# Kernel tuning notes

Hardware: AMD Instinct MI355X
Metric: run time of the kernel (lower is better)

The kernel has to match this reference:

```python
import jax, jax.numpy as jnp
import numpy as np

N, S, R, M, C, CZ = 1, 128, 256, 256, 32, 128


def setup_inputs() -> dict:
    key = jax.random.key(0)
    k1, k2, k3, k4 = jax.random.split(key, 4)
    return {
        "msa_repr": jax.random.normal(k1, (N, S, R, M), dtype=jnp.float32) * 0.1,
        "left_w": jax.random.normal(k2, (M, C), dtype=jnp.float32) * 0.02,
        "right_w": jax.random.normal(k3, (M, C), dtype=jnp.float32) * 0.02,
        "out_w": jax.random.normal(k4, (C * C, CZ), dtype=jnp.float32) * 0.02,
    }


def reference(msa_repr, left_w, right_w, out_w):
    # msa_repr: [N,S,R,M]
    n, s, r, m = msa_repr.shape
    c = left_w.shape[1]
    # opm_projection: [N,S,R,M] @ [M,C] -> [N,S,R,C]
    left = jnp.einsum('nsrm,mc->nsrc', msa_repr, left_w)
    right = jnp.einsum('nsrm,mc->nsrc', msa_repr, right_w)
    # outer product summed over MSA dim s: [N,R,T,C,C]
    # (torch: a=left.transpose(-2,-3) -> [N,R,S,C]; einsum '...bac,...dae->...bdce')
    outer = jnp.einsum('nsrc,nste->nrtce', left, right).reshape(n, r, r, c * c)
    # project to pair channel: [N,R,T,C*C] @ [C*C,CZ] -> [N,R,T,CZ]
    return jnp.matmul(outer, out_w)
```

## Files before the change

### kernel.cpp

```cpp
#include <hip/hip_runtime.h>
#include <stdint.h>

#define S_DIM 128
#define R_DIM 256
#define M_DIM 256
#define C_DIM 32
#define CZ_DIM 128
#define K2_DIM 1024

typedef _Float16 f16;
typedef _Float16 f16x4 __attribute__((ext_vector_type(4)));
typedef _Float16 f16x8 __attribute__((ext_vector_type(8)));
typedef float f32x4 __attribute__((ext_vector_type(4)));
typedef float f32x16 __attribute__((ext_vector_type(16)));

typedef const __attribute__((address_space(1))) uint32_t gu32_t;
typedef __attribute__((address_space(3))) uint32_t lu32_t;
#define GLOAD_LDS16(g, l) \
    __builtin_amdgcn_global_load_lds((gu32_t*)(g), (lu32_t*)(l), 16, 0, 0)

__global__ __launch_bounds__(256, 4)
void proj_kernel(const float* __restrict__ msa, const float* __restrict__ lw,
                 const float* __restrict__ rw, const float* __restrict__ ow,
                 f16* __restrict__ left_t, f16* __restrict__ rt2,
                 f16* __restrict__ wt2) {
    __shared__ __align__(16) f16 wlT[8192];
    __shared__ __align__(16) f16 wrT[8192];

    int bid = blockIdx.x;
    int tid = threadIdx.x;
    int w = tid >> 6;
    int lane = tid & 63;
    int q = lane >> 4, li = lane & 15;
    int r  = bid >> 1;
    int s0 = (bid & 1) << 6;
    int s_col = s0 + w * 16 + li;

    const f32x4* bp = (const f32x4*)(msa + ((size_t)s_col * R_DIM + r) * M_DIM + q * 8);
    f32x4 b[16];
#pragma unroll
    for (int ks = 0; ks < 8; ks++) { b[2 * ks] = bp[ks * 8]; b[2 * ks + 1] = bp[ks * 8 + 1]; }

    {
        int i = bid * 256 + tid;
        int cz = i >> 10, k2 = i & 1023;
        int c = k2 >> 5, e = k2 & 31;
        int k2p = ((e >> 2) << 7) + (c << 2) + (e & 3);
        int ntile = cz >> 5, l31o = cz & 31;
        int kk = k2p >> 4, q5o = (k2p >> 3) & 1, j = k2p & 7;
        wt2[(ntile * 64 + kk) * 512 + (l31o * 2 + q5o) * 8 + j] = (f16)ow[k2 * CZ_DIM + cz];
    }
#pragma unroll
    for (int k = 0; k < 32; k++) {
        int i = k * 256 + tid;
        int m = i >> 5, c = i & 31;
        int d = ((m >> 3) * 32 + c) * 8 + (m & 7);
        wlT[d] = (f16)lw[i];
        wrT[d] = (f16)rw[i];
    }
    __syncthreads();

    f32x4 aL0 = {0,0,0,0}, aL1 = {0,0,0,0}, aR0 = {0,0,0,0}, aR1 = {0,0,0,0};
#pragma unroll
    for (int ks = 0; ks < 8; ks++) {
        f16x8 bf;
#pragma unroll
        for (int u = 0; u < 4; u++) { bf[u] = (f16)b[2*ks][u]; bf[4 + u] = (f16)b[2*ks+1][u]; }
        const f16* a0 = wlT + ((ks * 4 + q) * 32 + li) * 8;
        const f16* a1 = wrT + ((ks * 4 + q) * 32 + li) * 8;
        f16x8 al0 = *(const f16x8*)(a0);
        f16x8 al1 = *(const f16x8*)(a0 + 128);
        f16x8 ar0 = *(const f16x8*)(a1);
        f16x8 ar1 = *(const f16x8*)(a1 + 128);
        aL0 = __builtin_amdgcn_mfma_f32_16x16x32_f16(al0, bf, aL0, 0, 0, 0);
        aL1 = __builtin_amdgcn_mfma_f32_16x16x32_f16(al1, bf, aL1, 0, 0, 0);
        aR0 = __builtin_amdgcn_mfma_f32_16x16x32_f16(ar0, bf, aR0, 0, 0, 0);
        aR1 = __builtin_amdgcn_mfma_f32_16x16x32_f16(ar1, bf, aR1, 0, 0, 0);
    }
    int ks_s = s_col >> 4, q5_s = (s_col >> 3) & 1, j_s = s_col & 7;
    int sbase = (r * 8 + ks_s) * 512 + q5_s * 8 + j_s;
    int rl = r & 7;
    f16* Lb = left_t + (size_t)(r >> 3) * 32768;
    int sc = s_col >> 3, sj = s_col & 7;
#pragma unroll
    for (int reg = 0; reg < 4; reg++) {
        int c0 = q * 4 + reg;
        int row0 = rl * 32 + c0;
        int swz = sc ^ c0;
        Lb[(row0 * 16 + swz) * 8 + sj]        = (f16)aL0[reg];
        Lb[((row0 + 16) * 16 + swz) * 8 + sj] = (f16)aL1[reg];
        rt2[sbase + c0 * 16]        = (f16)aR0[reg];
        rt2[sbase + (c0 + 16) * 16] = (f16)aR1[reg];
    }
}

__global__ __launch_bounds__(512, 2)
void fuse_kernel(const f16* __restrict__ left_t, const f16* __restrict__ rt2,
                 const f16* __restrict__ wt2, float* __restrict__ out) {
    extern __shared__ __align__(16) char lds[];
    f16* Ls = (f16*)lds;
    char* Pr = lds + 65536;

    int bid = blockIdx.x;
    int brq = bid >> 6, bt = bid & 63;
    int tid = threadIdx.x;
    int w = tid >> 6, lane = tid & 63;
    int q5 = lane >> 5, l31 = lane & 31, lx = lane & 15;

    int t_tile = w & 3, rg4 = w >> 2;
    int ntile = w & 3, kh = w >> 2;

    {
        const f16* Lg = left_t + (size_t)(brq * 4) * 32768;
#pragma unroll
        for (int it = 0; it < 8; it++)
            GLOAD_LDS16(Lg + (size_t)(it * 512 + tid) * 8, Ls + (it * 512 + tid) * 8);
    }

    int g = bt * 4 + t_tile;
    const f16* ap = rt2 + (size_t)g * 4096 + (l31 * 2 + q5) * 8;
    f16x8 afr[8];
#pragma unroll
    for (int ks = 0; ks < 8; ks++) afr[ks] = *(const f16x8*)(ap + ks * 512);

    const f16* wbase = wt2 + (size_t)(ntile * 64 + kh * 32) * 512 + (l31 * 2 + q5) * 8;
    const char* lbase = Pr + l31 * 2048;
    int base = 64 * kh + q5 + l31;

    f16x8 wfg[8][4];
#pragma unroll
    for (int u = 0; u < 4; u++) wfg[0][u] = *(const f16x8*)(wbase + u * 512);

    __syncthreads();

    for (int jr = 0; jr < 4; jr++) {
        int br = brq * 4 + jr;

        f32x16 acc[4] = {};
#pragma unroll
        for (int i = 0; i < 4; i++) {
            const f16* bbase = Ls + ((rg4 * 4 + i) * 32 + l31) * 128;
#pragma unroll
            for (int ks = 0; ks < 8; ks++) {
                f16x8 bfr = *(const f16x8*)(bbase + (((2 * ks + q5) ^ lx) << 3));
                acc[i] = __builtin_amdgcn_mfma_f32_32x32x16_f16(afr[ks], bfr, acc[i], 0, 0, 0);
            }
        }

        __syncthreads();

        int chc = l31 >> 1, bsub = 8 * (l31 & 1);
#pragma unroll
        for (int i = 0; i < 4; i++) {
            int p = (rg4 * 4 + i) * 4 + t_tile;
            char* prow = Pr + p * 2048;
#pragma unroll
            for (int rg = 0; rg < 4; rg++) {
                int ch = (2 * rg + q5) * 16 + chc;
                int phys = (ch + p) & 127;
                f16x4 h = {(f16)acc[i][4 * rg], (f16)acc[i][4 * rg + 1],
                           (f16)acc[i][4 * rg + 2], (f16)acc[i][4 * rg + 3]};
                *(f16x4*)(prow + phys * 16 + bsub) = h;
            }
        }
        __syncthreads();

        if (jr == 0) {
#pragma unroll
            for (int u = 0; u < 4; u++) wfg[1][u] = *(const f16x8*)(wbase + (4 + u) * 512);
#pragma unroll
            for (int u = 0; u < 4; u++) wfg[2][u] = *(const f16x8*)(wbase + (8 + u) * 512);
        }
        f16x8 afg[8][4];
#pragma unroll
        for (int u = 0; u < 4; u++)
            afg[0][u] = *(const f16x8*)(lbase + (((base + 2 * u) & 127) << 4));
#pragma unroll
        for (int u = 0; u < 4; u++)
            afg[1][u] = *(const f16x8*)(lbase + (((base + 8 + 2 * u) & 127) << 4));

        if (jr < 3) {
            const f16* Lg = left_t + (size_t)(br + 1) * 32768;
#pragma unroll
            for (int it = 0; it < 8; it++)
                GLOAD_LDS16(Lg + (size_t)(it * 512 + tid) * 8, Ls + (it * 512 + tid) * 8);
        }

        f32x16 accA = {}, accB = {};
#pragma unroll
        for (int gg = 0; gg < 8; gg++) {
            if (gg >= 1) {
                if (gg + 2 < 8) {
#pragma unroll
                    for (int u = 0; u < 4; u++)
                        wfg[gg + 2][u] = *(const f16x8*)(wbase + ((gg + 2) * 4 + u) * 512);
                }
                if (gg + 1 < 8) {
#pragma unroll
                    for (int u = 0; u < 4; u++)
                        afg[gg + 1][u] = *(const f16x8*)(lbase + (((base + (gg + 1) * 8 + 2 * u) & 127) << 4));
                }
            }
            accA = __builtin_amdgcn_mfma_f32_32x32x16_f16(afg[gg][0], wfg[gg][0], accA, 0, 0, 0);
            accB = __builtin_amdgcn_mfma_f32_32x32x16_f16(afg[gg][1], wfg[gg][1], accB, 0, 0, 0);
            accA = __builtin_amdgcn_mfma_f32_32x32x16_f16(afg[gg][2], wfg[gg][2], accA, 0, 0, 0);
            accB = __builtin_amdgcn_mfma_f32_32x32x16_f16(afg[gg][3], wfg[gg][3], accB, 0, 0, 0);
        }
        f32x16 acc2;
#pragma unroll
        for (int v = 0; v < 16; v++) acc2[v] = accA[v] + accB[v];
        __syncthreads();

        if (w >= 4) {
            char* rb = Pr + (w - 4) * 4096 + lane * 64;
#pragma unroll
            for (int u = 0; u < 4; u++) {
                f32x4 part = {acc2[4 * u], acc2[4 * u + 1], acc2[4 * u + 2], acc2[4 * u + 3]};
                *(f32x4*)(rb + u * 16) = part;
            }
        }
        __syncthreads();
        if (w < 4) {
            const char* rb = Pr + w * 4096 + lane * 64;
#pragma unroll
            for (int u = 0; u < 4; u++) {
                f32x4 part = *(const f32x4*)(rb + u * 16);
#pragma unroll
                for (int v = 0; v < 4; v++) acc2[4 * u + v] += part[v];
            }
            int r0 = br * 8, t0 = bt * 4, cz = w * 32 + l31;
#pragma unroll
            for (int reg = 0; reg < 16; reg++) {
                int p = (reg & 3) + 8 * (reg >> 2) + 4 * q5;
                out[((size_t)((r0 + (p >> 2)) * R_DIM + t0 + (p & 3))) * CZ_DIM + cz] = acc2[reg];
            }
        }
    }
}

extern "C" void kernel_launch(void* const* d_in, const int* in_sizes, int n_in,
                              void* d_out, int out_size, void* d_ws, size_t ws_size,
                              hipStream_t stream) {
    const float* msa = (const float*)d_in[0];
    const float* lw  = (const float*)d_in[1];
    const float* rw  = (const float*)d_in[2];
    const float* ow  = (const float*)d_in[3];
    char* ws = (char*)d_ws;
    f16* left_t = (f16*)(ws);
    f16* rt2    = (f16*)(ws + (size_t)2 * 1024 * 1024);
    f16* wt2    = (f16*)(ws + (size_t)4 * 1024 * 1024);
    float* out  = (float*)d_out;

    static bool attr_set = false;
    if (!attr_set) {
        hipFuncSetAttribute((const void*)fuse_kernel,
                            hipFuncAttributeMaxDynamicSharedMemorySize, 131072);
        attr_set = true;
    }

    proj_kernel<<<dim3(512), dim3(256), 0, stream>>>(msa, lw, rw, ow, left_t, rt2, wt2);
    fuse_kernel<<<dim3(512), dim3(512), 131072, stream>>>(left_t, rt2, wt2, out);
}
```

Measured before the change: 164.1 us.

## Process eight R rows per fuse block with swizzled block order and register-resident weights

Halves the fuse grid to 256 blocks, each looping over 8 rows instead of 4, and remaps block IDs so neighbouring blocks share a bt tile. The first two weight k-groups now stay in registers across iterations, the remaining weight fragments are loaded on a revised schedule, and the next left tile is prefetched earlier, right after the first MFMA phase. It also raises wave priority around the MFMA loops with s_setprio. Fewer blocks reduce per-block setup and reuse rt2/weight fragments more, but they cut parallelism on a GPU with 256 CUs and add register pressure.

Result: faster. 151.6 us (-7.6%).

```diff
diff --git a/kernel.cpp b/kernel.cpp
--- a/kernel.cpp
+++ b/kernel.cpp
@@ -101,42 +101,44 @@
     f16* Ls = (f16*)lds;
     char* Pr = lds + 65536;
 
-    int bid = blockIdx.x;
-    int brq = bid >> 6, bt = bid & 63;
+    int b = blockIdx.x;
+    int vb = (b & 7) * 32 + (b >> 3);
+    int brq = vb >> 6, bt = vb & 63;
     int tid = threadIdx.x;
     int w = tid >> 6, lane = tid & 63;
     int q5 = lane >> 5, l31 = lane & 31, lx = lane & 15;
 
     int t_tile = w & 3, rg4 = w >> 2;
-    int ntile = w & 3, kh = w >> 2;
+    int kh = w >> 2;
+    int chc = l31 >> 1, bsub = 8 * (l31 & 1);
 
     {
-        const f16* Lg = left_t + (size_t)(brq * 4) * 32768;
+        const f16* Lg = left_t + (size_t)(brq * 8) * 32768;
 #pragma unroll
         for (int it = 0; it < 8; it++)
             GLOAD_LDS16(Lg + (size_t)(it * 512 + tid) * 8, Ls + (it * 512 + tid) * 8);
     }
-
-    int g = bt * 4 + t_tile;
-    const f16* ap = rt2 + (size_t)g * 4096 + (l31 * 2 + q5) * 8;
+    const f16* ap = rt2 + (size_t)(bt * 4 + t_tile) * 4096 + (l31 * 2 + q5) * 8;
     f16x8 afr[8];
 #pragma unroll
     for (int ks = 0; ks < 8; ks++) afr[ks] = *(const f16x8*)(ap + ks * 512);
 
-    const f16* wbase = wt2 + (size_t)(ntile * 64 + kh * 32) * 512 + (l31 * 2 + q5) * 8;
+    const f16* wbase = wt2 + (size_t)(t_tile * 64 + kh * 32) * 512 + (l31 * 2 + q5) * 8;
+    f16x8 wR[8];
+#pragma unroll
+    for (int c = 0; c < 8; c++) wR[c] = *(const f16x8*)(wbase + c * 512);
+
     const char* lbase = Pr + l31 * 2048;
     int base = 64 * kh + q5 + l31;
 
-    f16x8 wfg[8][4];
-#pragma unroll
-    for (int u = 0; u < 4; u++) wfg[0][u] = *(const f16x8*)(wbase + u * 512);
-
     __syncthreads();
 
-    for (int jr = 0; jr < 4; jr++) {
-        int br = brq * 4 + jr;
+#pragma unroll 1
+    for (int j = 0; j < 8; j++) {
+        int br = brq * 8 + j;
 
         f32x16 acc[4] = {};
+        __builtin_amdgcn_s_setprio(1);
 #pragma unroll
         for (int i = 0; i < 4; i++) {
             const f16* bbase = Ls + ((rg4 * 4 + i) * 32 + l31) * 128;
@@ -146,10 +148,16 @@
                 acc[i] = __builtin_amdgcn_mfma_f32_32x32x16_f16(afr[ks], bfr, acc[i], 0, 0, 0);
             }
         }
-
-        __syncthreads();
-
-        int chc = l31 >> 1, bsub = 8 * (l31 & 1);
+        __builtin_amdgcn_s_setprio(0);
+        __syncthreads();
+
+        if (j < 7) {
+            const f16* Lg = left_t + (size_t)(br + 1) * 32768;
+#pragma unroll
+            for (int it = 0; it < 8; it++)
+                GLOAD_LDS16(Lg + (size_t)(it * 512 + tid) * 8, Ls + (it * 512 + tid) * 8);
+        }
+
 #pragma unroll
         for (int i = 0; i < 4; i++) {
             int p = (rg4 * 4 + i) * 4 + t_tile;
@@ -165,12 +173,11 @@
         }
         __syncthreads();
 
-        if (jr == 0) {
-#pragma unroll
-            for (int u = 0; u < 4; u++) wfg[1][u] = *(const f16x8*)(wbase + (4 + u) * 512);
-#pragma unroll
-            for (int u = 0; u < 4; u++) wfg[2][u] = *(const f16x8*)(wbase + (8 + u) * 512);
-        }
+        f16x8 wfs[8][4];
+#pragma unroll
+        for (int u = 0; u < 4; u++) wfs[2][u] = *(const f16x8*)(wbase + (8 + u) * 512);
+#pragma unroll
+        for (int u = 0; u < 4; u++) wfs[3][u] = *(const f16x8*)(wbase + (12 + u) * 512);
         f16x8 afg[8][4];
 #pragma unroll
         for (int u = 0; u < 4; u++)
@@ -179,33 +186,44 @@
         for (int u = 0; u < 4; u++)
             afg[1][u] = *(const f16x8*)(lbase + (((base + 8 + 2 * u) & 127) << 4));
 
-        if (jr < 3) {
-            const f16* Lg = left_t + (size_t)(br + 1) * 32768;
-#pragma unroll
-            for (int it = 0; it < 8; it++)
-                GLOAD_LDS16(Lg + (size_t)(it * 512 + tid) * 8, Ls + (it * 512 + tid) * 8);
-        }
-
         f32x16 accA = {}, accB = {};
+        __builtin_amdgcn_s_setprio(1);
 #pragma unroll
         for (int gg = 0; gg < 8; gg++) {
-            if (gg >= 1) {
-                if (gg + 2 < 8) {
-#pragma unroll
-                    for (int u = 0; u < 4; u++)
-                        wfg[gg + 2][u] = *(const f16x8*)(wbase + ((gg + 2) * 4 + u) * 512);
-                }
-                if (gg + 1 < 8) {
-#pragma unroll
-                    for (int u = 0; u < 4; u++)
-                        afg[gg + 1][u] = *(const f16x8*)(lbase + (((base + (gg + 1) * 8 + 2 * u) & 127) << 4));
-                }
-            }
-            accA = __builtin_amdgcn_mfma_f32_32x32x16_f16(afg[gg][0], wfg[gg][0], accA, 0, 0, 0);
-            accB = __builtin_amdgcn_mfma_f32_32x32x16_f16(afg[gg][1], wfg[gg][1], accB, 0, 0, 0);
-            accA = __builtin_amdgcn_mfma_f32_32x32x16_f16(afg[gg][2], wfg[gg][2], accA, 0, 0, 0);
-            accB = __builtin_amdgcn_mfma_f32_32x32x16_f16(afg[gg][3], wfg[gg][3], accB, 0, 0, 0);
-        }
+            if (gg == 1 || gg == 2 || gg == 3) {
+                int s = gg + 3;
+#pragma unroll
+                for (int u = 0; u < 4; u++)
+                    wfs[s][u] = *(const f16x8*)(wbase + (s * 4 + u) * 512);
+            }
+            if (gg == 5) {
+#pragma unroll
+                for (int u = 0; u < 4; u++)
+                    wfs[7][u] = *(const f16x8*)(wbase + (28 + u) * 512);
+            }
+            if (gg >= 1 && gg + 1 < 8) {
+#pragma unroll
+                for (int u = 0; u < 4; u++)
+                    afg[gg + 1][u] = *(const f16x8*)(lbase + (((base + (gg + 1) * 8 + 2 * u) & 127) << 4));
+            }
+            if (gg == 0) {
+                accA = __builtin_amdgcn_mfma_f32_32x32x16_f16(afg[gg][0], wR[0], accA, 0, 0, 0);
+                accB = __builtin_amdgcn_mfma_f32_32x32x16_f16(afg[gg][1], wR[1], accB, 0, 0, 0);
+                accA = __builtin_amdgcn_mfma_f32_32x32x16_f16(afg[gg][2], wR[2], accA, 0, 0, 0);
+                accB = __builtin_amdgcn_mfma_f32_32x32x16_f16(afg[gg][3], wR[3], accB, 0, 0, 0);
+            } else if (gg == 1) {
+                accA = __builtin_amdgcn_mfma_f32_32x32x16_f16(afg[gg][0], wR[4], accA, 0, 0, 0);
+                accB = __builtin_amdgcn_mfma_f32_32x32x16_f16(afg[gg][1], wR[5], accB, 0, 0, 0);
+                accA = __builtin_amdgcn_mfma_f32_32x32x16_f16(afg[gg][2], wR[6], accA, 0, 0, 0);
+                accB = __builtin_amdgcn_mfma_f32_32x32x16_f16(afg[gg][3], wR[7], accB, 0, 0, 0);
+            } else {
+                accA = __builtin_amdgcn_mfma_f32_32x32x16_f16(afg[gg][0], wfs[gg][0], accA, 0, 0, 0);
+                accB = __builtin_amdgcn_mfma_f32_32x32x16_f16(afg[gg][1], wfs[gg][1], accB, 0, 0, 0);
+                accA = __builtin_amdgcn_mfma_f32_32x32x16_f16(afg[gg][2], wfs[gg][2], accA, 0, 0, 0);
+                accB = __builtin_amdgcn_mfma_f32_32x32x16_f16(afg[gg][3], wfs[gg][3], accB, 0, 0, 0);
+            }
+        }
+        __builtin_amdgcn_s_setprio(0);
         f32x16 acc2;
 #pragma unroll
         for (int v = 0; v < 16; v++) acc2[v] = accA[v] + accB[v];
@@ -259,5 +277,5 @@
     }
 
     proj_kernel<<<dim3(512), dim3(256), 0, stream>>>(msa, lw, rw, ow, left_t, rt2, wt2);
-    fuse_kernel<<<dim3(512), dim3(512), 131072, stream>>>(left_t, rt2, wt2, out);
+    fuse_kernel<<<dim3(256), dim3(512), 131072, stream>>>(left_t, rt2, wt2, out);
 }
```
